# Optimization experiments

Measured on AMD Instinct MI355X. Metric: run time of the kernel, lower is better.

The kernel has to match this reference:

```python
import jax, jax.numpy as jnp
import numpy as np

B, H, W, D = 16, 32, 32, 256
K = 8192


def setup_inputs() -> dict:
    key = jax.random.key(0)
    k1, k2 = jax.random.split(key)
    z_e = jax.random.normal(k1, (B, H, W, D), dtype=jnp.float32)
    # flax nn.initializers.uniform(scale=1.0) -> U[0, 1)
    codebook = jax.random.uniform(k2, (K, D), dtype=jnp.float32)
    return {"z_e": z_e, "codebook": codebook}


def reference(z_e, codebook):
    b, h, w, d = z_e.shape
    z_flat = z_e.reshape(-1, d)  # (N, D)
    # squared-euclidean distances: ||z||^2 + ||e||^2 - 2 z.e  -> (N, K)
    z2 = jnp.sum(z_flat ** 2, axis=1, keepdims=True)
    e2 = jnp.sum(codebook ** 2, axis=1)[None, :]
    dist = z2 + e2 - 2.0 * (z_flat @ codebook.T)
    idx = jnp.argmin(dist, axis=1)  # (N,)
    z_q = codebook[idx].reshape(b, h, w, d)
    # straight-through estimator
    z_st = z_e + jax.lax.stop_gradient(z_q - z_e)
    commit = jnp.mean((jax.lax.stop_gradient(z_q) - z_e) ** 2)
    codebook_loss = jnp.mean((z_q - jax.lax.stop_gradient(z_e)) ** 2)
    return z_st, idx.reshape(b, h, w), commit, codebook_loss
```

## Files before the change

kernel.cpp:

```cpp
#include <hip/hip_runtime.h>

#define NROWS 16384
#define KCODES 8192
#define DDIM 256
#define MARGIN 1.0f
#define SEG 192
#define NCT 16
#define GATHER_BLOCKS (NROWS / 16)

typedef __attribute__((ext_vector_type(8))) short short8;
typedef __attribute__((ext_vector_type(4))) float f32x4;

__device__ inline unsigned short f2bf(float x) {
    unsigned u = __float_as_uint(x);
    return (unsigned short)((u + 0x7FFFu + ((u >> 16) & 1u)) >> 16);
}

__device__ inline void gload16(const void* g, void* l) {
    __builtin_amdgcn_global_load_lds(
        (const __attribute__((address_space(1))) unsigned char*)g,
        (__attribute__((address_space(3))) unsigned char*)l, 16, 0, 0);
}

__device__ inline unsigned mbcnt64(unsigned long long m) {
    unsigned lo = __builtin_amdgcn_mbcnt_lo((unsigned)m, 0u);
    return __builtin_amdgcn_mbcnt_hi((unsigned)(m >> 32), lo);
}

__device__ inline void exact_rescore(const float* __restrict__ z, const float* __restrict__ cb,
                                     const float* __restrict__ z2g, const float* __restrict__ e2g,
                                     int grow, int gcol, unsigned long long* best) {
    const float4* av = reinterpret_cast<const float4*>(z + (size_t)grow * DDIM);
    const float4* bv = reinterpret_cast<const float4*>(cb + (size_t)gcol * DDIM);
    float dot = 0.f;
    #pragma unroll 8
    for (int j = 0; j < 64; ++j) {
        const float4 xa = av[j], xb = bv[j];
        dot = fmaf(xa.x, xb.x, fmaf(xa.y, xb.y, fmaf(xa.z, xb.z, fmaf(xa.w, xb.w, dot))));
    }
    const float de = z2g[grow] + e2g[gcol] - 2.0f * dot;
    const unsigned long long key =
        ((unsigned long long)__float_as_uint(de) << 32) | (unsigned)gcol;
    atomicMin(best + grow, key);
}

__global__ __launch_bounds__(256) void k_convert(
    const float* __restrict__ cb, unsigned short* __restrict__ cb_t,
    float* __restrict__ e2,
    unsigned long long* best, float* accum, unsigned* counters, unsigned* gctr)
{
    const int tid = threadIdx.x;
    const int bx = blockIdx.x;
    if (bx < 64) {
        const int gid = bx * 256 + tid;
        best[gid] = 0xFFFFFFFFFFFFFFFFull;
    }
    if (bx == 0) {
        if (tid < 16) counters[tid * 16] = 0u;
        if (tid == 0) { accum[0] = 0.0f; gctr[0] = 0u; }
    }
    const int g = bx * 4 + (tid >> 6);
    const int lane = tid & 63;
    const int row = g * 16 + (lane & 15);
    const int ko = (lane >> 4) * 8;
    float ss = 0.f;
    #pragma unroll
    for (int kb2 = 0; kb2 < 8; ++kb2) {
        const float4* src = reinterpret_cast<const float4*>(cb + (size_t)row * DDIM + kb2 * 32 + ko);
        const float4 a = src[0], b = src[1];
        ss += a.x * a.x + a.y * a.y + a.z * a.z + a.w * a.w
            + b.x * b.x + b.y * b.y + b.z * b.z + b.w * b.w;
        short8 p;
        p[0] = (short)f2bf(a.x); p[1] = (short)f2bf(a.y); p[2] = (short)f2bf(a.z); p[3] = (short)f2bf(a.w);
        p[4] = (short)f2bf(b.x); p[5] = (short)f2bf(b.y); p[6] = (short)f2bf(b.z); p[7] = (short)f2bf(b.w);
        *reinterpret_cast<short8*>(cb_t + (((size_t)(g * 8 + kb2)) << 9) + lane * 8) = p;
    }
    ss += __shfl_xor(ss, 16);
    ss += __shfl_xor(ss, 32);
    if (lane < 16) e2[g * 16 + lane] = ss;
}

__global__ __launch_bounds__(1024, 4) void k_screen(
    const float* __restrict__ z, const float* __restrict__ cbp,
    const unsigned short* __restrict__ cb_t,
    float* z2g, const float* __restrict__ e2g,
    unsigned long long* __restrict__ best,
    unsigned* __restrict__ counters, unsigned* __restrict__ list, unsigned C16)
{
    __shared__ __align__(16) char smem[145664];
    char* ldsA = smem;
    char* ldsB = smem + 32768;
    float* rowmin = (float*)(smem + 131072);
    float* thrbuf = (float*)(smem + 133120);
    unsigned* wl_all = (unsigned*)(smem + 133376);

    const int tid = threadIdx.x;
    const int lane = tid & 63;
    const int wave = tid >> 6;
    const int wm = wave & 1;
    const int wn = wave >> 1;
    const int lhi = lane >> 4;
    const int llo = lane & 15;

    const int rt = blockIdx.x;
    const int row0 = rt * 64;

    auto STAGE_B = [&](int b, int ct_, int kb2_) {
        #pragma unroll
        for (int i = 0; i < 2; ++i) {
            const int c = wave * 2 + i;
            gload16((const char*)cb_t + (((size_t)((ct_ * 32 + c) * 8 + kb2_)) << 10) + lane * 16,
                    ldsB + b * 32768 + c * 1024);
        }
    };
    STAGE_B(0, 0, 0);
    STAGE_B(1, 0, 1);

    {
        const int c = tid >> 5;
        const int gl = c >> 3, kb2 = c & 7;
        const int sp = (tid & 31) * 2;
        #pragma unroll
        for (int i = 0; i < 2; ++i) {
            const int s = sp + i;
            const int row = gl * 16 + (s & 15);
            const int k = kb2 * 32 + (s >> 4) * 8;
            const float4* src = reinterpret_cast<const float4*>(z + (size_t)(row0 + row) * DDIM + k);
            const float4 a = src[0], b = src[1];
            short8 p;
            p[0] = (short)f2bf(a.x); p[1] = (short)f2bf(a.y); p[2] = (short)f2bf(a.z); p[3] = (short)f2bf(a.w);
            p[4] = (short)f2bf(b.x); p[5] = (short)f2bf(b.y); p[6] = (short)f2bf(b.z); p[7] = (short)f2bf(b.w);
            *reinterpret_cast<short8*>(ldsA + c * 1024 + s * 16) = p;
        }
    }

    #pragma unroll
    for (int rr = 0; rr < 4; ++rr) {
        const int row = wave * 4 + rr;
        const float4 v = *reinterpret_cast<const float4*>(z + (size_t)(row0 + row) * DDIM + lane * 4);
        float s = v.x * v.x + v.y * v.y + v.z * v.z + v.w * v.w;
        #pragma unroll
        for (int off = 1; off < 64; off <<= 1) s += __shfl_xor(s, off);
        if (lane == 0) z2g[row0 + row] = s;
    }

    if (tid < 64) thrbuf[tid] = 3.0e38f;
    __syncthreads();

    unsigned* wl = wl_all + wave * SEG;
    int S3 = 0;

    #pragma unroll 1
    for (int ci = 0; ci < NCT; ++ci) {
        f32x4 acc[2][4];
        #pragma unroll
        for (int i = 0; i < 2; ++i)
            #pragma unroll
            for (int j = 0; j < 4; ++j) { acc[i][j][0]=0.f; acc[i][j][1]=0.f; acc[i][j][2]=0.f; acc[i][j][3]=0.f; }

        #pragma unroll
        for (int kb2 = 0; kb2 < 8; ++kb2) {
            const int Sg = ci * 8 + kb2;
            int tb = S3 + 2; if (tb >= 3) tb -= 3;
            const int nS = Sg + 2;
            if (nS < NCT * 8) STAGE_B(tb, nS >> 3, nS & 7);

            char* bufB = ldsB + S3 * 32768;
            short8 bfr[4];
            #pragma unroll
            for (int fn = 0; fn < 4; ++fn)
                bfr[fn] = *reinterpret_cast<const short8*>(bufB + (wn * 4 + fn) * 1024 + lane * 16);
            #pragma unroll
            for (int fm = 0; fm < 2; ++fm) {
                const short8 af = *reinterpret_cast<const short8*>(
                    ldsA + (((wm * 2 + fm) * 8) + kb2) * 1024 + lane * 16);
                #pragma unroll
                for (int fn = 0; fn < 4; ++fn)
                    acc[fm][fn] = __builtin_amdgcn_mfma_f32_16x16x32_bf16(af, bfr[fn], acc[fm][fn], 0, 0, 0);
            }

            if (Sg >= NCT * 8 - 2) asm volatile("s_waitcnt vmcnt(0) lgkmcnt(0)" ::: "memory");
            else                   asm volatile("s_waitcnt vmcnt(2) lgkmcnt(0)" ::: "memory");
            __builtin_amdgcn_s_barrier();
            __builtin_amdgcn_sched_barrier(0);

            S3 = (S3 == 2) ? 0 : S3 + 1;
        }

        const int c0 = ci * 512 + wn * 64 + llo;
        float e2c[4];
        #pragma unroll
        for (int fn = 0; fn < 4; ++fn) e2c[fn] = e2g[c0 + fn * 16];

        #pragma unroll
        for (int fm = 0; fm < 2; ++fm) {
            #pragma unroll
            for (int rg = 0; rg < 4; ++rg) {
                const int rl = wm * 32 + fm * 16 + lhi * 4 + rg;
                float d[4];
                #pragma unroll
                for (int fn = 0; fn < 4; ++fn) d[fn] = fmaf(-2.0f, acc[fm][fn][rg], e2c[fn]);
                float m = fminf(fminf(d[0], d[1]), fminf(d[2], d[3]));
                #pragma unroll
                for (int off = 1; off < 16; off <<= 1) m = fminf(m, __shfl_xor(m, off));
                if (llo == 0) rowmin[wn * 64 + rl] = m;
            }
        }
        asm volatile("s_waitcnt lgkmcnt(0)" ::: "memory");
        __builtin_amdgcn_s_barrier();
        __builtin_amdgcn_sched_barrier(0);

        if (tid < 64) {
            float a = rowmin[tid];
            #pragma unroll
            for (int q = 1; q < 8; ++q) a = fminf(a, rowmin[q * 64 + tid]);
            thrbuf[tid] = fminf(thrbuf[tid], a);
        }
        asm volatile("s_waitcnt lgkmcnt(0)" ::: "memory");
        __builtin_amdgcn_s_barrier();
        __builtin_amdgcn_sched_barrier(0);

        unsigned wcount = 0;
        #pragma unroll
        for (int fm = 0; fm < 2; ++fm) {
            #pragma unroll
            for (int rg = 0; rg < 4; ++rg) {
                const int rl = wm * 32 + fm * 16 + lhi * 4 + rg;
                const float thr = thrbuf[rl] + MARGIN;
                float d[4];
                #pragma unroll
                for (int fn = 0; fn < 4; ++fn) d[fn] = fmaf(-2.0f, acc[fm][fn][rg], e2c[fn]);
                const bool hit = (d[0] <= thr) | (d[1] <= thr) | (d[2] <= thr) | (d[3] <= thr);
                if (__any(hit)) {
                    const int grow = row0 + rl;
                    #pragma unroll
                    for (int fn = 0; fn < 4; ++fn) {
                        const bool p = d[fn] <= thr;
                        const unsigned long long mask = __ballot(p);
                        if (mask) {
                            if (p) {
                                const unsigned pos = wcount + mbcnt64(mask);
                                const unsigned v = ((unsigned)grow << 13) | (unsigned)(c0 + fn * 16);
                                if (pos < SEG) wl[pos] = v;
                                else exact_rescore(z, cbp, z2g, e2g, grow, c0 + fn * 16, best);
                            }
                            wcount += (unsigned)__popcll(mask);
                        }
                    }
                }
            }
        }

        const unsigned n = wcount < SEG ? wcount : SEG;
        unsigned base = 0;
        if (lane == 0 && n) base = atomicAdd(&counters[wave * 16], n);
        base = (unsigned)__shfl((int)base, 0);
        for (unsigned i = lane; i < n; i += 64) {
            const unsigned v = wl[i];
            const unsigned slot = base + i;
            if (slot < C16) list[(size_t)wave * C16 + slot] = v;
            else exact_rescore(z, cbp, z2g, e2g, (int)(v >> 13), (int)(v & 8191u), best);
        }
    }
}

__global__ __launch_bounds__(256) void k_rescore(
    const float* __restrict__ z, const float* __restrict__ cbp,
    const float* __restrict__ z2g, const float* __restrict__ e2g,
    const unsigned* __restrict__ list, const unsigned* __restrict__ counters, unsigned C16,
    unsigned long long* best)
{
    const unsigned wid = (blockIdx.x * blockDim.x + threadIdx.x) >> 6;
    const unsigned nw = (gridDim.x * blockDim.x) >> 6;
    const int lane = threadIdx.x & 63;
    #pragma unroll 1
    for (int s = 0; s < 16; ++s) {
        const unsigned n = min(counters[s * 16], C16);
        const unsigned* shard = list + (size_t)s * C16;
        for (unsigned i = wid; i < n; i += nw) {
            const unsigned v = shard[i];
            const unsigned row = v >> 13, col = v & 8191u;
            const float4 a = *reinterpret_cast<const float4*>(z + (size_t)row * DDIM + lane * 4);
            const float4 b = *reinterpret_cast<const float4*>(cbp + (size_t)col * DDIM + lane * 4);
            float sdot = fmaf(a.x, b.x, fmaf(a.y, b.y, fmaf(a.z, b.z, a.w * b.w)));
            #pragma unroll
            for (int off = 1; off < 64; off <<= 1) sdot += __shfl_xor(sdot, off);
            if (lane == 0) {
                const float de = z2g[row] + e2g[col] - 2.0f * sdot;
                const unsigned long long key =
                    ((unsigned long long)__float_as_uint(de) << 32) | col;
                atomicMin(&best[row], key);
            }
        }
    }
}

__global__ __launch_bounds__(1024) void k_gather(
    const float* __restrict__ z, const float* __restrict__ cbp,
    const unsigned long long* __restrict__ best,
    float* __restrict__ out, float* __restrict__ accum, unsigned* __restrict__ gctr)
{
    __shared__ float wsum[16];
    const int tid = threadIdx.x;
    const int row = blockIdx.x * 16 + (tid >> 6);
    const int lane = tid & 63;
    const unsigned k = (unsigned)(best[row] & 0xFFFFFFFFull);
    const float4 ze = *reinterpret_cast<const float4*>(z + (size_t)row * DDIM + lane * 4);
    const float4 cq = *reinterpret_cast<const float4*>(cbp + (size_t)k * DDIM + lane * 4);
    float4 zst;
    zst.x = ze.x + (cq.x - ze.x); zst.y = ze.y + (cq.y - ze.y);
    zst.z = ze.z + (cq.z - ze.z); zst.w = ze.w + (cq.w - ze.w);
    *reinterpret_cast<float4*>(out + (size_t)row * DDIM + lane * 4) = zst;
    const float dx = cq.x - ze.x, dy = cq.y - ze.y, dz = cq.z - ze.z, dw = cq.w - ze.w;
    float s = dx * dx + dy * dy + dz * dz + dw * dw;
    #pragma unroll
    for (int off = 32; off > 0; off >>= 1) s += __shfl_down(s, off);
    if (lane == 0) {
        wsum[tid >> 6] = s;
        out[(size_t)NROWS * DDIM + row] = (float)k;
    }
    __syncthreads();
    if (tid == 0) {
        float tot = 0.f;
        #pragma unroll
        for (int i = 0; i < 16; ++i) tot += wsum[i];
        atomicAdd(accum, tot);
        __threadfence();
        const unsigned t = atomicAdd(gctr, 1u);
        if (t == GATHER_BLOCKS - 1) {
            const float total = atomicAdd(accum, 0.0f);
            const float m = total / (float)(NROWS * DDIM);
            out[(size_t)NROWS * DDIM + NROWS + 0] = m;
            out[(size_t)NROWS * DDIM + NROWS + 1] = m;
        }
    }
}

extern "C" void kernel_launch(void* const* d_in, const int* in_sizes, int n_in,
                              void* d_out, int out_size, void* d_ws, size_t ws_size,
                              hipStream_t stream)
{
    const float* z  = (const float*)d_in[0];
    const float* cb = (const float*)d_in[1];
    float* out = (float*)d_out;

    unsigned short* cb_t = (unsigned short*)d_out;

    char* ws = (char*)d_ws;
    unsigned long long* best = (unsigned long long*)ws;
    float* e2      = (float*)(ws + 131072);
    float* z2      = (float*)(ws + 163840);
    float* accum   = (float*)(ws + 229376);
    unsigned* gctr = (unsigned*)(ws + 229380);
    unsigned* counters = (unsigned*)(ws + 229440);
    unsigned* list = (unsigned*)(ws + 230464);
    unsigned C16 = 0;
    if (ws_size > 230464 + 64) {
        size_t c = (ws_size - 230464) / 4 / 16;
        if (c > (1u << 19)) c = (1u << 19);
        C16 = (unsigned)c;
    }

    k_convert<<<128, 256, 0, stream>>>(cb, cb_t, e2, best, accum, counters, gctr);
    k_screen<<<256, 1024, 0, stream>>>(z, cb, cb_t, z2, e2, best, counters, list, C16);
    k_rescore<<<1024, 256, 0, stream>>>(z, cb, z2, e2, list, counters, C16, best);
    k_gather<<<GATHER_BLOCKS, 1024, 0, stream>>>(z, cb, best, out, accum, gctr);
}
```

Baseline: 212.3 us.

## Load codebook fragments directly from global memory instead of LDS triple buffering

Removes the triple-buffered LDS staging of codebook tiles via global_load_lds and the per-step barriers. Each wave now reads its B fragments straight from global memory into registers. This cuts LDS use sharply, which may allow more blocks per CU, and drops the synchronisation. In exchange it gives up the prefetch overlap, and every wave re-fetches the same data through the cache.

```diff
diff --git a/kernel.cpp b/kernel.cpp
--- a/kernel.cpp
+++ b/kernel.cpp
@@ -14,12 +14,6 @@
 __device__ inline unsigned short f2bf(float x) {
     unsigned u = __float_as_uint(x);
     return (unsigned short)((u + 0x7FFFu + ((u >> 16) & 1u)) >> 16);
-}
-
-__device__ inline void gload16(const void* g, void* l) {
-    __builtin_amdgcn_global_load_lds(
-        (const __attribute__((address_space(1))) unsigned char*)g,
-        (__attribute__((address_space(3))) unsigned char*)l, 16, 0, 0);
 }
 
 __device__ inline unsigned mbcnt64(unsigned long long m) {
@@ -87,12 +81,11 @@
     unsigned long long* __restrict__ best,
     unsigned* __restrict__ counters, unsigned* __restrict__ list, unsigned C16)
 {
-    __shared__ __align__(16) char smem[145664];
+    __shared__ __align__(16) char smem[47360];
     char* ldsA = smem;
-    char* ldsB = smem + 32768;
-    float* rowmin = (float*)(smem + 131072);
-    float* thrbuf = (float*)(smem + 133120);
-    unsigned* wl_all = (unsigned*)(smem + 133376);
+    float* rowmin = (float*)(smem + 32768);
+    float* thrbuf = (float*)(smem + 34816);
+    unsigned* wl_all = (unsigned*)(smem + 35072);
 
     const int tid = threadIdx.x;
     const int lane = tid & 63;
@@ -104,17 +97,6 @@
 
     const int rt = blockIdx.x;
     const int row0 = rt * 64;
-
-    auto STAGE_B = [&](int b, int ct_, int kb2_) {
-        #pragma unroll
-        for (int i = 0; i < 2; ++i) {
-            const int c = wave * 2 + i;
-            gload16((const char*)cb_t + (((size_t)((ct_ * 32 + c) * 8 + kb2_)) << 10) + lane * 16,
-                    ldsB + b * 32768 + c * 1024);
-        }
-    };
-    STAGE_B(0, 0, 0);
-    STAGE_B(1, 0, 1);
 
     {
         const int c = tid >> 5;
@@ -148,7 +130,6 @@
     __syncthreads();
 
     unsigned* wl = wl_all + wave * SEG;
-    int S3 = 0;
 
     #pragma unroll 1
     for (int ci = 0; ci < NCT; ++ci) {
@@ -158,18 +139,13 @@
             #pragma unroll
             for (int j = 0; j < 4; ++j) { acc[i][j][0]=0.f; acc[i][j][1]=0.f; acc[i][j][2]=0.f; acc[i][j][3]=0.f; }
 
+        const char* bbase = (const char*)cb_t + (((size_t)((ci * 32 + wn * 4)) * 8) << 10) + lane * 16;
         #pragma unroll
         for (int kb2 = 0; kb2 < 8; ++kb2) {
-            const int Sg = ci * 8 + kb2;
-            int tb = S3 + 2; if (tb >= 3) tb -= 3;
-            const int nS = Sg + 2;
-            if (nS < NCT * 8) STAGE_B(tb, nS >> 3, nS & 7);
-
-            char* bufB = ldsB + S3 * 32768;
             short8 bfr[4];
             #pragma unroll
             for (int fn = 0; fn < 4; ++fn)
-                bfr[fn] = *reinterpret_cast<const short8*>(bufB + (wn * 4 + fn) * 1024 + lane * 16);
+                bfr[fn] = *reinterpret_cast<const short8*>(bbase + fn * 8192 + kb2 * 1024);
             #pragma unroll
             for (int fm = 0; fm < 2; ++fm) {
                 const short8 af = *reinterpret_cast<const short8*>(
@@ -178,13 +154,6 @@
                 for (int fn = 0; fn < 4; ++fn)
                     acc[fm][fn] = __builtin_amdgcn_mfma_f32_16x16x32_bf16(af, bfr[fn], acc[fm][fn], 0, 0, 0);
             }
-
-            if (Sg >= NCT * 8 - 2) asm volatile("s_waitcnt vmcnt(0) lgkmcnt(0)" ::: "memory");
-            else                   asm volatile("s_waitcnt vmcnt(2) lgkmcnt(0)" ::: "memory");
-            __builtin_amdgcn_s_barrier();
-            __builtin_amdgcn_sched_barrier(0);
-
-            S3 = (S3 == 2) ? 0 : S3 + 1;
         }
 
         const int c0 = ci * 512 + wn * 64 + llo;
```

Result: no change. 210.0 us, median of 3 (-1.1%).
